# Optimization experiments

Measured on AMD Instinct MI355X. Metric: run time of the kernel, lower is better.

Reference implementation:

```python
import jax, jax.numpy as jnp
import numpy as np
from jax import lax

B, N, T = 64, 50, 30          # batch, history length, words per title
VOCAB, E = 50000, 300          # vocab size, word emb dim
FN, A, G, K = 400, 200, 400, 3 # filter_num, attention_dim, gru_unit, window size
USERS = 50000


def setup_inputs() -> dict:
    key = jax.random.key(0)
    ks = jax.random.split(key, 12)
    return {
        "user_id": jax.random.randint(ks[0], (B,), 0, USERS),
        "history_title": jax.random.randint(ks[1], (B, N, T), 0, VOCAB),
        "history_length": jax.random.randint(ks[2], (B,), 1, N + 1),
        "word_emb": jax.random.normal(ks[3], (VOCAB, E), jnp.float32) * 0.02,
        "conv_w": jax.random.normal(ks[4], (K, E, FN), jnp.float32) * 0.05,  # WIO layout
        "conv_b": jnp.zeros((FN,), jnp.float32),
        "v": jax.random.normal(ks[5], (FN, A), jnp.float32) * 0.05,
        "vb": jnp.zeros((A,), jnp.float32),
        "q": jax.random.normal(ks[6], (A, 1), jnp.float32) * 0.05,
        "user_emb": jax.random.normal(ks[7], (USERS, G), jnp.float32) * 0.02,
        "W_ih": jax.random.normal(ks[8], (3 * G, FN), jnp.float32) * 0.05,
        "W_hh": jax.random.normal(ks[9], (3 * G, G), jnp.float32) * 0.05,
        "b_ih": jnp.zeros((3 * G,), jnp.float32),
        "b_hh": jnp.zeros((3 * G,), jnp.float32),
    }


def _news_encode(history_title, word_emb, conv_w, conv_b, v, vb, q):
    # word embedding lookup: [B, N, T, E] (dropout is identity in eval mode)
    W = word_emb[history_title]
    # Conv1d over the word axis, padding=1 keeps length T
    x = W.reshape(B * N, T, E)
    C = lax.conv_general_dilated(
        x, conv_w, window_strides=(1,), padding=[(1, 1)],
        dimension_numbers=("NWC", "WIO", "NWC")) + conv_b
    C = jax.nn.relu(C).reshape(B, N, T, FN)
    # additive attention scores
    a = jnp.tanh(jnp.einsum("bntf,fa->bnta", C, v) + vb)
    a = jnp.einsum("bnta,ao->bnt", a, q)  # q: [A,1] -> squeeze
    # original uses Softmax(dim=0) on a [n, t] per sample => over the n-titles axis
    alpha = jax.nn.softmax(a, axis=1)
    # e[i] = alpha[i] @ C[i]: weighted sum over words -> [B, N, FN]
    return jnp.einsum("bnt,bntf->bnf", alpha, C)


def _gru(news_embed, h0, lengths, W_ih, W_hh, b_ih, b_hh):
    # packed_padded semantics: h stops updating once step >= length
    xs = jnp.swapaxes(news_embed, 0, 1)                 # [N, B, FN]
    mask = jnp.arange(N)[:, None] < lengths[None, :]    # [N, B]

    def step(h, inp):
        x_t, m = inp
        gx = x_t @ W_ih.T + b_ih                        # [B, 3G]
        gh = h @ W_hh.T + b_hh
        xr, xz, xn = jnp.split(gx, 3, axis=-1)
        hr, hz, hn = jnp.split(gh, 3, axis=-1)
        r = jax.nn.sigmoid(xr + hr)
        z = jax.nn.sigmoid(xz + hz)
        n = jnp.tanh(xn + r * hn)
        h_new = (1.0 - z) * n + z * h
        h = jnp.where(m[:, None], h_new, h)
        return h, None

    h_final, _ = lax.scan(step, h0, (xs, mask))
    return h_final


def reference(user_id, history_title, history_length, word_emb, conv_w, conv_b,
              v, vb, q, user_emb, W_ih, W_hh, b_ih, b_hh):
    news_embed = _news_encode(history_title, word_emb, conv_w, conv_b, v, vb, q)
    h0 = user_emb[user_id]                              # [B, G]
    return _gru(news_embed, h0, history_length, W_ih, W_hh, b_ih, b_hh)
```

## Files before the change

kernel.cpp:

```cpp
#include <hip/hip_runtime.h>
#include <hip/hip_bf16.h>

#define BB 64
#define NN 50
#define TT 30
#define EE 300
#define FN 400
#define AA 200
#define GG 400

typedef __attribute__((ext_vector_type(8))) short bf16x8;
typedef __attribute__((ext_vector_type(4))) float f32x4;

__device__ inline ushort f2bf(float x) {
  __hip_bfloat16 b = __float2bfloat16(x);
  return *(ushort*)&b;
}

__global__ void k_prep_all(
    const float* __restrict__ Whh, const float* __restrict__ cw,
    const float* __restrict__ v, const float* __restrict__ q,
    const float* __restrict__ vb, const float* __restrict__ Wih,
    const int* __restrict__ user_id, const float* __restrict__ user_emb,
    float* __restrict__ Wpack, __hip_bfloat16* __restrict__ WT2,
    __hip_bfloat16* __restrict__ vT2, float* __restrict__ qp,
    float* __restrict__ vbp, __hip_bfloat16* __restrict__ Wih_bf,
    float* __restrict__ h0)
{
  int i = blockIdx.x * 256 + threadIdx.x;
  if (i < 480000) {
    int jl = i % 150;
    int g = (i / 150) % 400;
    int gc = i / 60000;
    int gate = jl / 50, gl = jl - gate * 50;
    int j = gate * 400 + gc * 50 + gl;
    Wpack[i] = Whh[j * 400 + g];
  } else if (i < 910080) {
    int k = i - 480000;
    int kk = k & 31, f = (k >> 5) % 448, s = k / (448 * 32);
    int ko = s / 10, e = (s - ko * 10) * 32 + kk;
    float val = (f < FN && e < EE) ? cw[(ko * EE + e) * FN + f] : 0.f;
    WT2[k] = __float2bfloat16(val);
  } else if (i < 1003264) {
    int k = i - 910080;
    int kk = k & 31, a = (k >> 5) % 224, ks = k / (224 * 32);
    int e = ks * 32 + kk;
    float val = (a < AA && e < FN) ? v[e * AA + a] : 0.f;
    vT2[k] = __float2bfloat16(val);
  } else if (i < 1003488) {
    int k = i - 1003264;
    qp[k]  = k < AA ? q[k]  : 0.f;
    vbp[k] = k < AA ? vb[k] : 0.f;
  } else if (i < 1562592) {
    int k = i - 1003488;
    int j = k / 416, f = k % 416;
    Wih_bf[k] = __float2bfloat16((j < 1200 && f < FN) ? Wih[j * 400 + f] : 0.f);
  } else if (i < 1588192) {
    int k = i - 1562592;
    int b = k / GG, g = k - b * GG;
    h0[k] = user_emb[(size_t)user_id[b] * GG + g];
  }
}

__global__ __launch_bounds__(256, 2) void k_conv(
    const int* __restrict__ title, const float* __restrict__ word_emb,
    const __hip_bfloat16* __restrict__ WT2, const float* __restrict__ conv_b,
    __hip_bfloat16* __restrict__ C)
{
  __shared__ __align__(16) ushort E[2][34][344];
  __shared__ int words[60];
  const int g = blockIdx.x;
  const int tid = threadIdx.x;
  const int lane = tid & 63, wn = tid >> 6;
  const int l15 = lane & 15, l4 = lane >> 4;

  if (tid < 60) words[tid] = title[g * 60 + tid];
  for (int idx = tid; idx < 2924; idx += 256)
    *(uint4*)((ushort*)E + idx * 8) = make_uint4(0u, 0u, 0u, 0u);
  __syncthreads();
  for (int idx = tid; idx < 4500; idx += 256) {
    int row = idx / 75, ch = idx - row * 75;
    int tt = row / 30, w = row - tt * 30;
    float4 v4 = *(const float4*)(word_emb + (size_t)words[row] * EE + ch * 4);
    ushort4 u4 = make_ushort4(f2bf(v4.x), f2bf(v4.y), f2bf(v4.z), f2bf(v4.w));
    *(ushort4*)(&E[tt][w + 1][ch * 4]) = u4;
  }
  __syncthreads();

  f32x4 acc[4][7];
#pragma unroll
  for (int nt = 0; nt < 7; ++nt) {
    int f = wn * 112 + nt * 16 + l15;
    float bj = (f < FN) ? conv_b[f] : 0.f;
#pragma unroll
    for (int mt = 0; mt < 4; ++mt) {
      acc[mt][nt][0] = bj; acc[mt][nt][1] = bj;
      acc[mt][nt][2] = bj; acc[mt][nt][3] = bj;
    }
  }

  const ushort* Bbase = (const ushort*)WT2 + (size_t)(wn * 112 + l15) * 32 + l4 * 8;

#define LOADB(dst, s) {                                                        \
    const ushort* p_ = Bbase + (size_t)(s) * 14336;                            \
    _Pragma("unroll")                                                          \
    for (int nt = 0; nt < 7; ++nt) dst[nt] = *(const bf16x8*)(p_ + nt * 512);  \
  }
#define DOMFMA(bq, s) {                                                        \
    const int ko_ = (s) / 10, ks_ = (s) % 10;                                  \
    bf16x8 af_[4];                                                             \
    _Pragma("unroll")                                                          \
    for (int mt = 0; mt < 4; ++mt)                                             \
      af_[mt] = *(const bf16x8*)(&E[mt >> 1][(mt & 1) * 16 + l15 + ko_]        \
                                   [ks_ * 32 + l4 * 8]);                       \
    _Pragma("unroll")                                                          \
    for (int nt = 0; nt < 7; ++nt)                                             \
      _Pragma("unroll")                                                        \
      for (int mt = 0; mt < 4; ++mt)                                           \
        acc[mt][nt] = __builtin_amdgcn_mfma_f32_16x16x32_bf16(                 \
            af_[mt], bq[nt], acc[mt][nt], 0, 0, 0);                            \
  }

  bf16x8 bqA[7], bqB[7];
  LOADB(bqA, 0);
#pragma unroll
  for (int it = 0; it < 15; ++it) {
    const int s0 = it * 2;
    LOADB(bqB, s0 + 1);
    DOMFMA(bqA, s0);
    if (it < 14) LOADB(bqA, s0 + 2);
    DOMFMA(bqB, s0 + 1);
  }
#undef LOADB
#undef DOMFMA

#pragma unroll
  for (int mt = 0; mt < 4; ++mt) {
    const int ti = mt >> 1;
    const int tb = (mt & 1) * 16 + l4 * 4;
#pragma unroll
    for (int nt = 0; nt < 7; ++nt) {
      int f = wn * 112 + nt * 16 + l15;
      if (f < 416) {
#pragma unroll
        for (int r = 0; r < 4; ++r) {
          int t = tb + r;
          if (t < TT) {
            float vv = fmaxf(acc[mt][nt][r], 0.f);
            C[((size_t)(g * 2 + ti) * 30 + t) * 416 + f] = __float2bfloat16(vv);
          }
        }
      }
    }
  }
}

__global__ __launch_bounds__(512) void k_attn(
    const __hip_bfloat16* __restrict__ C, const __hip_bfloat16* __restrict__ vT2,
    const float* __restrict__ vbp, const float* __restrict__ qp,
    float* __restrict__ score)
{
  __shared__ __align__(16) ushort Clds[256 * 40];
  __shared__ float sred[2][256];
  const int tid = threadIdx.x;
  const int lane = tid & 63, wid = tid >> 6;
  const int wm = wid >> 1, wn = wid & 1;
  const int l15 = lane & 15, l4 = lane >> 4;
  const size_t row0 = (size_t)blockIdx.x * 256;

  f32x4 acc[4][7];
  float ql[7];
#pragma unroll
  for (int nt = 0; nt < 7; ++nt) {
    int a = wn * 112 + nt * 16 + l15;
    ql[nt] = qp[a];
    float vbv = vbp[a];
#pragma unroll
    for (int mt = 0; mt < 4; ++mt) {
      acc[mt][nt][0] = vbv; acc[mt][nt][1] = vbv;
      acc[mt][nt][2] = vbv; acc[mt][nt][3] = vbv;
    }
  }

  const ushort* Vbase = (const ushort*)vT2 + (size_t)(wn * 112 + l15) * 32 + l4 * 8;

  for (int ks = 0; ks < 13; ++ks) {
    bf16x8 vf[7];
#pragma unroll
    for (int nt = 0; nt < 7; ++nt)
      vf[nt] = *(const bf16x8*)(Vbase + ((size_t)ks * 224 + nt * 16) * 32);
    for (int idx = tid; idx < 1024; idx += 512) {
      int r = idx >> 2, c = idx & 3;
      *(uint4*)(&Clds[r * 40 + c * 8]) =
          *(const uint4*)((const ushort*)C + (row0 + r) * 416 + ks * 32 + c * 8);
    }
    __syncthreads();
    bf16x8 cf[4];
#pragma unroll
    for (int mt = 0; mt < 4; ++mt)
      cf[mt] = *(const bf16x8*)(&Clds[(wm * 64 + mt * 16 + l15) * 40 + l4 * 8]);
#pragma unroll
    for (int nt = 0; nt < 7; ++nt)
#pragma unroll
      for (int mt = 0; mt < 4; ++mt)
        acc[mt][nt] = __builtin_amdgcn_mfma_f32_16x16x32_bf16(cf[mt], vf[nt], acc[mt][nt], 0, 0, 0);
    __syncthreads();
  }

  float sums[4][4];
#pragma unroll
  for (int mt = 0; mt < 4; ++mt)
#pragma unroll
    for (int r = 0; r < 4; ++r) sums[mt][r] = 0.f;
#pragma unroll
  for (int mt = 0; mt < 4; ++mt)
#pragma unroll
    for (int nt = 0; nt < 7; ++nt)
#pragma unroll
      for (int r = 0; r < 4; ++r)
        sums[mt][r] += tanhf(acc[mt][nt][r]) * ql[nt];
#pragma unroll
  for (int mask = 1; mask < 16; mask <<= 1)
#pragma unroll
    for (int mt = 0; mt < 4; ++mt)
#pragma unroll
      for (int r = 0; r < 4; ++r)
        sums[mt][r] += __shfl_xor(sums[mt][r], mask);

  float outv = 0.f;
#pragma unroll
  for (int mt = 0; mt < 4; ++mt)
#pragma unroll
    for (int r = 0; r < 4; ++r)
      if (l15 == mt * 4 + r) outv = sums[mt][r];
  sred[wn][wm * 64 + (l15 >> 2) * 16 + l4 * 4 + (l15 & 3)] = outv;
  __syncthreads();
  if (tid < 256) score[row0 + tid] = sred[0][tid] + sred[1][tid];
}

__global__ void k2_softmax_n(const float* __restrict__ score, float* __restrict__ alpha) {
  int i = blockIdx.x * 256 + threadIdx.x;
  if (i >= BB * TT) return;
  int b = i / TT, t = i - b * TT;
  int base = b * (NN * TT) + t;
  float m = -1e30f;
  for (int n = 0; n < NN; ++n) m = fmaxf(m, score[base + n * TT]);
  float s = 0.f;
  for (int n = 0; n < NN; ++n) s += __expf(score[base + n * TT] - m);
  float inv = 1.f / s;
  for (int n = 0; n < NN; ++n)
    alpha[base + n * TT] = __expf(score[base + n * TT] - m) * inv;
}

__global__ __launch_bounds__(256) void k3_wsum(
    const float* __restrict__ alpha, const __hip_bfloat16* __restrict__ C,
    __hip_bfloat16* __restrict__ Ebf) {
  __shared__ float al[TT];
  const int bn = blockIdx.x;
  const int tid = threadIdx.x;
  if (tid < TT) al[tid] = alpha[bn * TT + tid];
  __syncthreads();
  for (int f = tid; f < 416; f += 256) {
    float s = 0.f;
    if (f < FN) {
#pragma unroll
      for (int t = 0; t < TT; ++t)
        s = fmaf(al[t], __bfloat162float(C[((size_t)bn * TT + t) * 416 + f]), s);
    }
    Ebf[(size_t)bn * 416 + f] = __float2bfloat16(s);
  }
}

__global__ __launch_bounds__(512) void k4_gx_mfma(
    const __hip_bfloat16* __restrict__ Ebf,
    const __hip_bfloat16* __restrict__ Wih,
    const float* __restrict__ b_ih,
    float* __restrict__ gx)
{
  __shared__ __align__(16) ushort Alds[128 * 40];
  __shared__ __align__(16) ushort Blds[448 * 40];
  const int tid = threadIdx.x;
  const int lane = tid & 63, wid = tid >> 6;
  const int wm = wid >> 2, wn = wid & 3;
  const int l15 = lane & 15, l4 = lane >> 4;
  const int mb = blockIdx.x / 3;
  const int nb = blockIdx.x - mb * 3;
  const int row0 = mb * 128;
  const int n0 = nb * 448;

  f32x4 acc[4][7];
#pragma unroll
  for (int nt = 0; nt < 7; ++nt) {
    int j = n0 + wn * 112 + nt * 16 + l15;
    float bj = (j < 1200) ? b_ih[j] : 0.f;
#pragma unroll
    for (int mt = 0; mt < 4; ++mt) {
      acc[mt][nt][0] = bj; acc[mt][nt][1] = bj;
      acc[mt][nt][2] = bj; acc[mt][nt][3] = bj;
    }
  }

  const int ar = tid >> 2, ac = tid & 3;
  for (int ks = 0; ks < 13; ++ks) {
    *(uint4*)(&Alds[ar * 40 + ac * 8]) =
        *(const uint4*)((const ushort*)Ebf + (size_t)(row0 + ar) * 416 + ks * 32 + ac * 8);
    for (int idx = tid; idx < 1792; idx += 512) {
      int r = idx >> 2, c = idx & 3;
      *(uint4*)(&Blds[r * 40 + c * 8]) =
          *(const uint4*)((const ushort*)Wih + (size_t)(n0 + r) * 416 + ks * 32 + c * 8);
    }
    __syncthreads();
    bf16x8 af[4];
#pragma unroll
    for (int mt = 0; mt < 4; ++mt)
      af[mt] = *(const bf16x8*)(&Alds[(wm * 64 + mt * 16 + l15) * 40 + l4 * 8]);
#pragma unroll
    for (int nt = 0; nt < 7; ++nt) {
      bf16x8 bfr = *(const bf16x8*)(&Blds[(wn * 112 + nt * 16 + l15) * 40 + l4 * 8]);
#pragma unroll
      for (int mt = 0; mt < 4; ++mt)
        acc[mt][nt] = __builtin_amdgcn_mfma_f32_16x16x32_bf16(af[mt], bfr, acc[mt][nt], 0, 0, 0);
    }
    __syncthreads();
  }

#pragma unroll
  for (int mt = 0; mt < 4; ++mt) {
    int row = row0 + wm * 64 + mt * 16 + l4 * 4;
#pragma unroll
    for (int nt = 0; nt < 7; ++nt) {
      int j = n0 + wn * 112 + nt * 16 + l15;
      if (j < 1200) {
#pragma unroll
        for (int r = 0; r < 4; ++r)
          gx[(size_t)(row + r) * 1200 + j] = acc[mt][nt][r];
      }
    }
  }
}

__global__ __launch_bounds__(256) void k5_step(
    const float* __restrict__ h_prev, float* __restrict__ h_next,
    const float* __restrict__ Wpack, const float* __restrict__ b_hh,
    const float* __restrict__ gx, const int* __restrict__ hist_len,
    float* __restrict__ out, int step)
{
  const int gc = blockIdx.x & 7;
  const int bg = blockIdx.x >> 3;
  const int tid = threadIdx.x;
  __shared__ float hl[2][GG];
  __shared__ float ghl[2][3][50];

  for (int i = tid; i < 2 * GG; i += 256) {
    int b = i / GG, g = i - b * GG;
    hl[b][g] = h_prev[(2 * bg + b) * GG + g];
  }
  __syncthreads();

  if (tid < 150) {
    float a00 = 0.f, a01 = 0.f, a10 = 0.f, a11 = 0.f;
    const float* wp = Wpack + (size_t)gc * 60000 + tid;
#pragma unroll 4
    for (int g = 0; g < 200; ++g) {
      float w0 = wp[g * 150];
      float w1 = wp[(g + 200) * 150];
      a00 = fmaf(hl[0][g], w0, a00);
      a10 = fmaf(hl[1][g], w0, a10);
      a01 = fmaf(hl[0][g + 200], w1, a01);
      a11 = fmaf(hl[1][g + 200], w1, a11);
    }
    int gate = tid / 50, gl = tid - gate * 50;
    float bb = b_hh[gate * 400 + gc * 50 + gl];
    ghl[0][gate][gl] = a00 + a01 + bb;
    ghl[1][gate][gl] = a10 + a11 + bb;
  }
  __syncthreads();

  if (tid < 100) {
    int b = tid / 50, gl = tid - (tid / 50) * 50;
    int babs = 2 * bg + b;
    int g = gc * 50 + gl;
    const float* gxp = gx + ((size_t)babs * NN + step) * 1200;
    float xr = gxp[g], xz = gxp[400 + g], xn = gxp[800 + g];
    float hr = ghl[b][0][gl], hz = ghl[b][1][gl], hn = ghl[b][2][gl];
    float r = 1.f / (1.f + __expf(-(xr + hr)));
    float z = 1.f / (1.f + __expf(-(xz + hz)));
    float nv = tanhf(xn + r * hn);
    float hold = hl[b][g];
    float hnew = (1.f - z) * nv + z * hold;
    float hres = (step < hist_len[babs]) ? hnew : hold;
    h_next[babs * GG + g] = hres;
    if (step == NN - 1) out[babs * GG + g] = hres;
  }
}

extern "C" void kernel_launch(void* const* d_in, const int* in_sizes, int n_in,
                              void* d_out, int out_size, void* d_ws, size_t ws_size,
                              hipStream_t stream) {
  const int*   user_id   = (const int*)d_in[0];
  const int*   title     = (const int*)d_in[1];
  const int*   hist_len  = (const int*)d_in[2];
  const float* word_emb  = (const float*)d_in[3];
  const float* conv_w    = (const float*)d_in[4];
  const float* conv_b    = (const float*)d_in[5];
  const float* v         = (const float*)d_in[6];
  const float* vb        = (const float*)d_in[7];
  const float* q         = (const float*)d_in[8];
  const float* user_emb  = (const float*)d_in[9];
  const float* W_ih      = (const float*)d_in[10];
  const float* W_hh      = (const float*)d_in[11];
  const float* b_ih      = (const float*)d_in[12];
  const float* b_hh      = (const float*)d_in[13];
  float* out = (float*)d_out;

  char* ws = (char*)d_ws;
  size_t off = 0;
  auto take = [&](size_t bytes) {
    char* p = ws + off;
    off = (off + bytes + 255) & ~(size_t)255;
    return p;
  };
  __hip_bfloat16* C      = (__hip_bfloat16*)take((size_t)BB * NN * TT * 416 * 2);
  float* score  = (float*)take((size_t)BB * NN * TT * 4);
  float* alpha  = (float*)take((size_t)BB * NN * TT * 4);
  __hip_bfloat16* Ebf    = (__hip_bfloat16*)take((size_t)BB * NN * 416 * 2);
  __hip_bfloat16* Wih_bf = (__hip_bfloat16*)take((size_t)1344 * 416 * 2);
  float* Wpack  = (float*)take((size_t)8 * 400 * 150 * 4);
  float* gx     = (float*)take((size_t)BB * NN * 1200 * 4);
  float* h0     = (float*)take((size_t)BB * GG * 4);
  float* h1     = (float*)take((size_t)BB * GG * 4);
  __hip_bfloat16* WT2    = (__hip_bfloat16*)take((size_t)30 * 448 * 32 * 2);
  __hip_bfloat16* vT2    = (__hip_bfloat16*)take((size_t)13 * 224 * 32 * 2);
  float* qp     = (float*)take(224 * 4);
  float* vbp    = (float*)take(224 * 4);
  (void)ws_size;

  k_prep_all<<<6204, 256, 0, stream>>>(W_hh, conv_w, v, q, vb, W_ih, user_id,
                                       user_emb, Wpack, WT2, vT2, qp, vbp,
                                       Wih_bf, h0);

  k_conv<<<BB * NN / 2, 256, 0, stream>>>(title, word_emb, WT2, conv_b, C);
  k_attn<<<BB * NN * TT / 256, 512, 0, stream>>>(C, vT2, vbp, qp, score);
  k2_softmax_n<<<(BB * TT + 255) / 256, 256, 0, stream>>>(score, alpha);
  k3_wsum<<<BB * NN, 256, 0, stream>>>(alpha, C, Ebf);
  k4_gx_mfma<<<75, 512, 0, stream>>>(Ebf, Wih_bf, b_ih, gx);

  float* hbuf[2] = {h0, h1};
  for (int step = 0; step < NN; ++step) {
    k5_step<<<256, 256, 0, stream>>>(hbuf[step & 1], hbuf[(step + 1) & 1],
                                     Wpack, b_hh, gx, hist_len, out, step);
  }
}
```

Measured before the change: 882.0 us.

## Pre-convert word embeddings to bf16, drop LDS staging in attn and GRU step

Adds a kernel that converts the whole 50000x300 fp32 embedding table to a padded bf16 table on every call, so the conv gather reads half the bytes with wider loads. k_attn now loads C fragments straight from global memory with nontemporal loads instead of staging through LDS with barriers, and k_conv writes C with nontemporal stores. k5_step reads h_prev directly from global memory instead of copying it into shared memory, and the unroll factor goes from 4 to 8. Converting the full table costs roughly 60MB of reads plus 32MB of writes per call, while the gather only touches about 96k rows, so the extra kernel may cost more than it saves.

```diff
diff --git a/kernel.cpp b/kernel.cpp
--- a/kernel.cpp
+++ b/kernel.cpp
@@ -62,8 +62,21 @@
   }
 }
 
+__global__ void k_prep_emb(const float* __restrict__ w, __hip_bfloat16* __restrict__ o) {
+  int i = blockIdx.x * 256 + threadIdx.x;
+  if (i < 50000 * 80) {
+    int row = i / 80, cg = i - row * 80;
+    ushort4 u4 = make_ushort4(0, 0, 0, 0);
+    if (cg < 75) {
+      float4 v4 = *(const float4*)(w + (size_t)row * EE + cg * 4);
+      u4 = make_ushort4(f2bf(v4.x), f2bf(v4.y), f2bf(v4.z), f2bf(v4.w));
+    }
+    *(ushort4*)((ushort*)o + (size_t)row * 320 + cg * 4) = u4;
+  }
+}
+
 __global__ __launch_bounds__(256, 2) void k_conv(
-    const int* __restrict__ title, const float* __restrict__ word_emb,
+    const int* __restrict__ title, const __hip_bfloat16* __restrict__ emb,
     const __hip_bfloat16* __restrict__ WT2, const float* __restrict__ conv_b,
     __hip_bfloat16* __restrict__ C)
 {
@@ -78,12 +91,11 @@
   for (int idx = tid; idx < 2924; idx += 256)
     *(uint4*)((ushort*)E + idx * 8) = make_uint4(0u, 0u, 0u, 0u);
   __syncthreads();
-  for (int idx = tid; idx < 4500; idx += 256) {
-    int row = idx / 75, ch = idx - row * 75;
+  for (int idx = tid; idx < 2400; idx += 256) {
+    int row = idx / 40, c = idx - row * 40;
     int tt = row / 30, w = row - tt * 30;
-    float4 v4 = *(const float4*)(word_emb + (size_t)words[row] * EE + ch * 4);
-    ushort4 u4 = make_ushort4(f2bf(v4.x), f2bf(v4.y), f2bf(v4.z), f2bf(v4.w));
-    *(ushort4*)(&E[tt][w + 1][ch * 4]) = u4;
+    *(uint4*)(&E[tt][w + 1][c * 8]) =
+        *(const uint4*)((const ushort*)emb + (size_t)words[row] * 320 + c * 8);
   }
   __syncthreads();
 
@@ -146,8 +158,9 @@
         for (int r = 0; r < 4; ++r) {
           int t = tb + r;
           if (t < TT) {
-            float vv = fmaxf(acc[mt][nt][r], 0.f);
-            C[((size_t)(g * 2 + ti) * 30 + t) * 416 + f] = __float2bfloat16(vv);
+            ushort us = f2bf(fmaxf(acc[mt][nt][r], 0.f));
+            __builtin_nontemporal_store(
+                us, (ushort*)C + ((size_t)(g * 2 + ti) * 30 + t) * 416 + f);
           }
         }
       }
@@ -160,7 +173,6 @@
     const float* __restrict__ vbp, const float* __restrict__ qp,
     float* __restrict__ score)
 {
-  __shared__ __align__(16) ushort Clds[256 * 40];
   __shared__ float sred[2][256];
   const int tid = threadIdx.x;
   const int lane = tid & 63, wid = tid >> 6;
@@ -183,28 +195,23 @@
   }
 
   const ushort* Vbase = (const ushort*)vT2 + (size_t)(wn * 112 + l15) * 32 + l4 * 8;
+  const ushort* Cbase = (const ushort*)C + (row0 + wm * 64 + l15) * 416 + l4 * 8;
 
   for (int ks = 0; ks < 13; ++ks) {
     bf16x8 vf[7];
 #pragma unroll
     for (int nt = 0; nt < 7; ++nt)
       vf[nt] = *(const bf16x8*)(Vbase + ((size_t)ks * 224 + nt * 16) * 32);
-    for (int idx = tid; idx < 1024; idx += 512) {
-      int r = idx >> 2, c = idx & 3;
-      *(uint4*)(&Clds[r * 40 + c * 8]) =
-          *(const uint4*)((const ushort*)C + (row0 + r) * 416 + ks * 32 + c * 8);
-    }
-    __syncthreads();
     bf16x8 cf[4];
 #pragma unroll
     for (int mt = 0; mt < 4; ++mt)
-      cf[mt] = *(const bf16x8*)(&Clds[(wm * 64 + mt * 16 + l15) * 40 + l4 * 8]);
+      cf[mt] = __builtin_nontemporal_load(
+          (const bf16x8*)(Cbase + (size_t)mt * 16 * 416 + ks * 32));
 #pragma unroll
     for (int nt = 0; nt < 7; ++nt)
 #pragma unroll
       for (int mt = 0; mt < 4; ++mt)
         acc[mt][nt] = __builtin_amdgcn_mfma_f32_16x16x32_bf16(cf[mt], vf[nt], acc[mt][nt], 0, 0, 0);
-    __syncthreads();
   }
 
   float sums[4][4];
@@ -348,26 +355,23 @@
   const int gc = blockIdx.x & 7;
   const int bg = blockIdx.x >> 3;
   const int tid = threadIdx.x;
-  __shared__ float hl[2][GG];
   __shared__ float ghl[2][3][50];
 
-  for (int i = tid; i < 2 * GG; i += 256) {
-    int b = i / GG, g = i - b * GG;
-    hl[b][g] = h_prev[(2 * bg + b) * GG + g];
-  }
-  __syncthreads();
-
   if (tid < 150) {
+    const float* h0p = h_prev + (size_t)(2 * bg) * GG;
+    const float* h1p = h0p + GG;
     float a00 = 0.f, a01 = 0.f, a10 = 0.f, a11 = 0.f;
     const float* wp = Wpack + (size_t)gc * 60000 + tid;
-#pragma unroll 4
+#pragma unroll 8
     for (int g = 0; g < 200; ++g) {
       float w0 = wp[g * 150];
       float w1 = wp[(g + 200) * 150];
-      a00 = fmaf(hl[0][g], w0, a00);
-      a10 = fmaf(hl[1][g], w0, a10);
-      a01 = fmaf(hl[0][g + 200], w1, a01);
-      a11 = fmaf(hl[1][g + 200], w1, a11);
+      float h00 = h0p[g], h01 = h0p[g + 200];
+      float h10 = h1p[g], h11 = h1p[g + 200];
+      a00 = fmaf(h00, w0, a00);
+      a10 = fmaf(h10, w0, a10);
+      a01 = fmaf(h01, w1, a01);
+      a11 = fmaf(h11, w1, a11);
     }
     int gate = tid / 50, gl = tid - gate * 50;
     float bb = b_hh[gate * 400 + gc * 50 + gl];
@@ -386,11 +390,11 @@
     float r = 1.f / (1.f + __expf(-(xr + hr)));
     float z = 1.f / (1.f + __expf(-(xz + hz)));
     float nv = tanhf(xn + r * hn);
-    float hold = hl[b][g];
+    float hold = h_prev[(size_t)babs * GG + g];
     float hnew = (1.f - z) * nv + z * hold;
     float hres = (step < hist_len[babs]) ? hnew : hold;
-    h_next[babs * GG + g] = hres;
-    if (step == NN - 1) out[babs * GG + g] = hres;
+    h_next[(size_t)babs * GG + g] = hres;
+    if (step == NN - 1) out[(size_t)babs * GG + g] = hres;
   }
 }
 
@@ -429,6 +433,7 @@
   float* gx     = (float*)take((size_t)BB * NN * 1200 * 4);
   float* h0     = (float*)take((size_t)BB * GG * 4);
   float* h1     = (float*)take((size_t)BB * GG * 4);
+  __hip_bfloat16* emb_bf = (__hip_bfloat16*)take((size_t)50000 * 320 * 2);
   __hip_bfloat16* WT2    = (__hip_bfloat16*)take((size_t)30 * 448 * 32 * 2);
   __hip_bfloat16* vT2    = (__hip_bfloat16*)take((size_t)13 * 224 * 32 * 2);
   float* qp     = (float*)take(224 * 4);
@@ -438,8 +443,9 @@
   k_prep_all<<<6204, 256, 0, stream>>>(W_hh, conv_w, v, q, vb, W_ih, user_id,
                                        user_emb, Wpack, WT2, vT2, qp, vbp,
                                        Wih_bf, h0);
-
-  k_conv<<<BB * NN / 2, 256, 0, stream>>>(title, word_emb, WT2, conv_b, C);
+  k_prep_emb<<<(50000 * 80 + 255) / 256, 256, 0, stream>>>(word_emb, emb_bf);
+
+  k_conv<<<BB * NN / 2, 256, 0, stream>>>(title, emb_bf, WT2, conv_b, C);
   k_attn<<<BB * NN * TT / 256, 512, 0, stream>>>(C, vT2, vbp, qp, score);
   k2_softmax_n<<<(BB * TT + 255) / 256, 256, 0, stream>>>(score, alpha);
   k3_wsum<<<BB * NN, 256, 0, stream>>>(alpha, C, Ebf);
```

New measurement: 990.9 us. +12.3%, slower.
